# Kernel optimization log

Hardware: AMD Instinct MI355X
Metric: run time of the kernel (lower is better)

Reference implementation:

```python
import jax, jax.numpy as jnp
import numpy as np

B, S, D, H = 4, 2048, 1024, 16
PD = D // H  # projection (head) dim


def setup_inputs() -> dict:
    key = jax.random.key(0)
    ks = jax.random.split(key, 11)
    s = 1.0 / np.sqrt(D)
    return {
        "q": jax.random.normal(ks[0], (B, S, D), jnp.float32),
        "k": jax.random.normal(ks[1], (B, S, D), jnp.float32),
        "v": jax.random.normal(ks[2], (B, S, D), jnp.float32),
        "Wq": jax.random.normal(ks[3], (D, D), jnp.float32) * s,
        "bq": jnp.zeros((D,), jnp.float32),
        "Wk": jax.random.normal(ks[4], (D, D), jnp.float32) * s,
        "bk": jnp.zeros((D,), jnp.float32),
        "Wv": jax.random.normal(ks[5], (D, D), jnp.float32) * s,
        "bv": jnp.zeros((D,), jnp.float32),
        "Wo": jax.random.normal(ks[6], (D, D), jnp.float32) * s,
        "bo": jnp.zeros((D,), jnp.float32),
        "use_causal_mask": 1,
    }


def _split_heads(x):
    # [B,S,D] -> [B,H,S,PD]
    return x.reshape(B, S, H, PD).transpose(0, 2, 1, 3)


def reference(q, k, v, Wq, bq, Wk, bk, Wv, bv, Wo, bo, use_causal_mask):
    qh = _split_heads(q @ Wq + bq)
    kh = _split_heads(k @ Wk + bk)
    vh = _split_heads(v @ Wv + bv)
    # scaled dot-product attention, O(S^2) scores materialized as in original
    logits = jnp.einsum("bhsd,bhtd->bhst", qh, kh) / jnp.sqrt(jnp.float32(PD))
    if use_causal_mask:
        # Faithful to original (buggy) mask: band_part lower-tri ones, then
        # logits += log(mask*1e-6 + 1.0) -- adds ~1e-6 where allowed, 0 where masked.
        mask = jnp.tril(jnp.ones((S, S), jnp.float32))
        logits = logits + jnp.log(mask * 1e-6 + 1.0)
    attn = jax.nn.softmax(logits, axis=-1)
    out = jnp.einsum("bhst,bhtd->bhsd", attn, vh)
    concat = out.transpose(0, 2, 1, 3).reshape(B, S, D)
    return concat @ Wo + bo
```

## Files before the change

kernel.cpp:

```cpp
#include <hip/hip_runtime.h>

#define B_ 4
#define S_ 2048
#define D_ 1024
#define H_ 16
#define PD_ 64
#define M_ 8192
#define QSCALE 0.180336880145787f

typedef __attribute__((ext_vector_type(8))) short s16x8;
typedef __attribute__((ext_vector_type(4))) short s16x4;
typedef __attribute__((ext_vector_type(4))) float f32x4;

__device__ __forceinline__ short f2bf(float f) {
    unsigned int u = __float_as_uint(f);
    u = (u + 0x7FFFu + ((u >> 16) & 1u)) >> 16;
    return (short)u;
}

__device__ __forceinline__ unsigned int cvt_pk_bf16(float lo, float hi) {
    unsigned int r;
    asm("v_cvt_pk_bf16_f32 %0, %1, %2" : "=v"(r) : "v"(lo), "v"(hi));
    return r;
}

#if __has_builtin(__builtin_amdgcn_exp2f)
__device__ __forceinline__ float fast_exp2(float x) { return __builtin_amdgcn_exp2f(x); }
#else
__device__ __forceinline__ float fast_exp2(float x) {
    float r;
    asm("v_exp_f32 %0, %1" : "=v"(r) : "v"(x));
    return r;
}
#endif

#define MFMA(a, b, c) __builtin_amdgcn_mfma_f32_16x16x32_bf16(a, b, c, 0, 0, 0)

#if __has_builtin(__builtin_amdgcn_mfma_f32_16x16x16bf16_1k)
__device__ __forceinline__ f32x4 MFMA16(s16x4 a, s16x4 b, f32x4 c) {
    return __builtin_amdgcn_mfma_f32_16x16x16bf16_1k(a, b, c, 0, 0, 0);
}
#elif __has_builtin(__builtin_amdgcn_mfma_f32_16x16x16_bf16)
typedef __attribute__((ext_vector_type(4))) __bf16 bf16x4;
__device__ __forceinline__ f32x4 MFMA16(s16x4 a, s16x4 b, f32x4 c) {
    union UA { s16x4 s; bf16x4 b; };
    UA ua, ub;
    ua.s = a; ub.s = b;
    return __builtin_amdgcn_mfma_f32_16x16x16_bf16(ua.b, ub.b, c, 0, 0, 0);
}
#else
__device__ __forceinline__ f32x4 MFMA16(s16x4 a, s16x4 b, f32x4 c) {
    asm volatile("s_nop 1\n\tv_mfma_f32_16x16x16_bf16 %0, %1, %2, %0\n\ts_nop 7\n\ts_nop 7"
                 : "+v"(c) : "v"(a), "v"(b));
    return c;
}
#endif

__device__ __forceinline__ void gload16(const short* g, short* l) {
    __builtin_amdgcn_global_load_lds(
        (const __attribute__((address_space(1))) void*)g,
        (__attribute__((address_space(3))) void*)l, 16, 0, 0);
}

__global__ __launch_bounds__(256) void cvt_kernel(
    const float* __restrict__ q, const float* __restrict__ k, const float* __restrict__ v,
    short* __restrict__ oq, short* __restrict__ ok, short* __restrict__ ov) {
    const int z = blockIdx.z;
    const float* X = (z == 0) ? q : (z == 1) ? k : v;
    short* out = (z == 0) ? oq : (z == 1) ? ok : ov;
    const float s = (z == 0) ? QSCALE : 1.0f;
    size_t i0 = ((size_t)blockIdx.x * 256 + threadIdx.x) * 8;
    const size_t stride = (size_t)1024 * 256 * 8;
#pragma unroll
    for (int it = 0; it < 4; it++, i0 += stride) {
        float4 f0 = *(const float4*)&X[i0];
        float4 f1 = *(const float4*)&X[i0 + 4];
        s16x8 o = {f2bf(f0.x * s), f2bf(f0.y * s), f2bf(f0.z * s), f2bf(f0.w * s),
                   f2bf(f1.x * s), f2bf(f1.y * s), f2bf(f1.z * s), f2bf(f1.w * s)};
        *(s16x8*)&out[i0] = o;
    }
}

__global__ void wt_kernel(const float* __restrict__ Wq, const float* __restrict__ Wk,
                          const float* __restrict__ Wv, const float* __restrict__ Wo,
                          short* __restrict__ wt) {
    const float* W = (blockIdx.z == 0) ? Wq : (blockIdx.z == 1) ? Wk
                     : (blockIdx.z == 2) ? Wv : Wo;
    short* out = wt + (size_t)blockIdx.z * (D_ * D_);
    __shared__ float tile[32][33];
    const int k0 = blockIdx.x * 32, n0 = blockIdx.y * 32;
    const int tx = threadIdx.x, ty = threadIdx.y;
#pragma unroll
    for (int i = 0; i < 4; i++)
        tile[ty + 8 * i][tx] = W[(size_t)(k0 + ty + 8 * i) * D_ + n0 + tx];
    __syncthreads();
#pragma unroll
    for (int i = 0; i < 4; i++)
        out[(size_t)(n0 + ty + 8 * i) * D_ + k0 + tx] = f2bf(tile[tx][ty + 8 * i]);
}

__device__ __forceinline__ void gemm_core(const short* __restrict__ A,
                                          const short* __restrict__ Bm,
                                          int bm, int bn, short* lds,
                                          f32x4 acc[4][4]) {
    const int tid = threadIdx.x;
    const int lane = tid & 63, wid = tid >> 6;
    const int wr = (wid >> 1) * 64, wc = (wid & 1) * 64;
    const int l15 = lane & 15, l4 = lane >> 4;

    const int rr = tid >> 2;
    const int cc = tid & 3;
    const int csw = (cc ^ ((rr >> 1) & 3)) * 8;
    const short* ap = A + (size_t)(bm + rr) * D_ + csw;
    const short* bp = Bm + (size_t)(bn + rr) * D_ + csw;
    const int ldw = wid * 512;

    const int ard = (l4 ^ ((l15 >> 1) & 3)) * 8;

#define PSTAGE(bi, kkc)                                                  \
    do {                                                                 \
        short* Lp = lds + (bi) * 8192;                                   \
        gload16(ap + (kkc), Lp + ldw);                                   \
        gload16(ap + (size_t)64 * D_ + (kkc), Lp + 2048 + ldw);          \
        gload16(bp + (kkc), Lp + 4096 + ldw);                            \
        gload16(bp + (size_t)64 * D_ + (kkc), Lp + 6144 + ldw);          \
    } while (0)

    PSTAGE(0, 0);
    PSTAGE(1, 32);

    int cur = 0;
    for (int t = 0; t < 32; t++) {
        if (t + 2 < 32) {
            int nb = cur + 2;
            if (nb >= 3) nb -= 3;
            PSTAGE(nb, (t + 2) * 32);
        }
        if (t <= 29)
            asm volatile("s_waitcnt vmcnt(8)" ::: "memory");
        else if (t == 30)
            asm volatile("s_waitcnt vmcnt(4)" ::: "memory");
        else
            asm volatile("s_waitcnt vmcnt(0)" ::: "memory");
        __builtin_amdgcn_s_barrier();

        const short* La = lds + cur * 8192;
        const short* Lb = La + 4096;
        s16x8 af[4], bf[4];
#pragma unroll
        for (int i = 0; i < 4; i++)
            af[i] = *(const s16x8*)&La[(wr + i * 16 + l15) * 32 + ard];
#pragma unroll
        for (int j = 0; j < 4; j++)
            bf[j] = *(const s16x8*)&Lb[(wc + j * 16 + l15) * 32 + ard];
#pragma unroll
        for (int i = 0; i < 4; i++)
#pragma unroll
            for (int j = 0; j < 4; j++)
                acc[i][j] = MFMA(bf[j], af[i], acc[i][j]);

        __builtin_amdgcn_s_barrier();
        cur = (cur == 2) ? 0 : cur + 1;
    }
#undef PSTAGE
}

__global__ __launch_bounds__(256) void proj_kernel(
    const short* __restrict__ xq, const short* __restrict__ xk, const short* __restrict__ xv,
    const float* __restrict__ bq, const float* __restrict__ bk, const float* __restrict__ bv,
    const short* __restrict__ wtbase, short* __restrict__ outQ, short* __restrict__ outK,
    short* __restrict__ outVT) {
    const int id = blockIdx.x;
    const int xcd = id & 7, slot = id >> 3;
    const int sb = xcd + 8 * (slot >> 6);
    const int wi = slot & 63;
    const int z = sb >> 3;
    const int bn = (wi & 7) * 128;
    const int bm = (((sb & 7) << 3) + (wi >> 3)) * 128;

    const short* A = (z == 0) ? xq : (z == 1) ? xk : xv;
    const float* bias = (z == 0) ? bq : (z == 1) ? bk : bv;
    const short* Wt = wtbase + (size_t)z * (D_ * D_);
    const float bscale = (z == 0) ? QSCALE : 1.0f;

    __shared__ __align__(16) short lds[3 * 8192];

    const int tid = threadIdx.x;
    const int lane = tid & 63, wid = tid >> 6;
    const int wr = (wid >> 1) * 64, wc = (wid & 1) * 64;
    const int l15 = lane & 15, l4 = lane >> 4;

    f32x4 acc[4][4];
#pragma unroll
    for (int i = 0; i < 4; i++)
#pragma unroll
        for (int j = 0; j < 4; j++) acc[i][j] = (f32x4){0.f, 0.f, 0.f, 0.f};

    gemm_core(A, Wt, bm, bn, lds, acc);

    if (z == 2) {
        const int b = bm >> 11, sbase = bm & (S_ - 1);
        short* T = lds;
        for (int chunk = 0; chunk < 4; chunk++) {
            __syncthreads();
            if ((wc >> 6) == (chunk >> 1)) {
                const int jbase = (chunk & 1) * 2;
#pragma unroll
                for (int jj = 0; jj < 2; jj++) {
                    const int j = jbase + jj;
                    float4 b4 = *(const float4*)&bias[bn + wc + j * 16 + l4 * 4];
                    const int prow = jj * 16 + l4 * 4;
#pragma unroll
                    for (int i = 0; i < 4; i++) {
                        const int sc2 = wr + i * 16 + l15;
                        T[(prow + 0) * 132 + sc2] = f2bf(acc[i][j][0] + b4.x);
                        T[(prow + 1) * 132 + sc2] = f2bf(acc[i][j][1] + b4.y);
                        T[(prow + 2) * 132 + sc2] = f2bf(acc[i][j][2] + b4.z);
                        T[(prow + 3) * 132 + sc2] = f2bf(acc[i][j][3] + b4.w);
                    }
                }
            }
            __syncthreads();
#pragma unroll
            for (int pass = 0; pass < 2; pass++) {
                const int r = pass * 16 + (tid >> 4);
                const int sc3 = (tid & 15) * 8;
                s16x8 vv = *(const s16x8*)&T[r * 132 + sc3];
                const int grow = b * 1024 + bn + chunk * 32 + r;
                const int kvg = sc3 & 64;
                const int c8 = (sc3 >> 3) & 7;
                const int posA = ((2 * c8) & 3) * 16 + (c8 >> 1) * 4;
                const int posB = ((2 * c8 + 1) & 3) * 16 + (c8 >> 1) * 4;
                const int sx = (r & 7) << 3;
                const s16x4* hv = (const s16x4*)&vv;
                const size_t base = (size_t)grow * S_ + sbase + kvg;
                *(s16x4*)&outVT[base + (posA ^ sx)] = hv[0];
                *(s16x4*)&outVT[base + (posB ^ sx)] = hv[1];
            }
        }
    } else {
        short* out = (z == 0) ? outQ : outK;
#pragma unroll
        for (int i = 0; i < 4; i++) {
            const int m = bm + wr + i * 16 + l15;
            const int b = m >> 11, s = m & (S_ - 1);
#pragma unroll
            for (int j = 0; j < 4; j++) {
                const int n = bn + wc + j * 16 + l4 * 4;
                float4 b4 = *(const float4*)&bias[n];
                s16x4 st;
                st[0] = f2bf(acc[i][j][0] + b4.x * bscale);
                st[1] = f2bf(acc[i][j][1] + b4.y * bscale);
                st[2] = f2bf(acc[i][j][2] + b4.z * bscale);
                st[3] = f2bf(acc[i][j][3] + b4.w * bscale);
                const int h = n >> 6, pd = n & 63;
                const int pdsw = (z == 1) ? (pd ^ ((s & 7) << 3)) : pd;
                *(s16x4*)&out[(((size_t)(b * H_ + h)) * S_ + s) * PD_ + pdsw] = st;
            }
        }
    }
}

__global__ __launch_bounds__(512, 4) void attn_kernel(
    const short* __restrict__ Qh, const short* __restrict__ Kh,
    const short* __restrict__ Vtg, short* __restrict__ aout) {
    const int did = blockIdx.x + gridDim.x * blockIdx.y;
    const int bh = (did & 7) * 8 + ((did >> 3) & 7);
    const int q0 = (did >> 6) * 128;
    const short* Qp = Qh + (size_t)bh * (S_ * PD_);
    const short* Kp = Kh + (size_t)bh * (S_ * PD_);
    const short* Vp = Vtg + (size_t)bh * (PD_ * S_);

    const int tid = threadIdx.x;
    const int lane = tid & 63, w = tid >> 6;
    const int l15 = lane & 15, l4 = lane >> 4;
    const int swz = (l15 & 7) << 3;

    __shared__ __align__(16) short Ks[3][64 * 64];
    __shared__ __align__(16) short Vs[3][64 * 64];

    s16x8 qf[2];
#pragma unroll
    for (int kk = 0; kk < 2; kk++)
        qf[kk] = *(const s16x8*)&Qp[(size_t)(q0 + w * 16 + l15) * PD_ + kk * 32 + l4 * 8];

    const s16x4 ones = {(short)0x3F80, (short)0x3F80, (short)0x3F80, (short)0x3F80};

    f32x4 oacc[4];
#pragma unroll
    for (int i = 0; i < 4; i++) oacc[i] = (f32x4){0.f, 0.f, 0.f, 0.f};
    f32x4 sacc = (f32x4){0.f, 0.f, 0.f, 0.f};

    const short* kbase = Kp + (size_t)(tid >> 3) * PD_ + (tid & 7) * 8;
    const short* vbase = Vp + (size_t)(tid >> 3) * S_ + (tid & 7) * 8;
    const int ldw = w * 512;

#define AISSUE(bsel, st)                                              \
    do {                                                              \
        gload16(kbase + (size_t)(st) * (64 * PD_), &Ks[bsel][ldw]);   \
        gload16(vbase + (st) * 64, &Vs[bsel][ldw]);                   \
    } while (0)

    AISSUE(0, 0);
    AISSUE(1, 1);

    int cur = 0;
    for (int t = 0; t < 32; t++) {
        if (t < 31)
            asm volatile("s_waitcnt vmcnt(2)" ::: "memory");
        else
            asm volatile("s_waitcnt vmcnt(0)" ::: "memory");
        __syncthreads();
        if (t + 2 < 32) {
            int nb = cur + 2;
            if (nb >= 3) nb -= 3;
            AISSUE(nb, t + 2);
        }
        const short* Kc = Ks[cur];
        const short* Vc = Vs[cur];

        f32x4 s4[4];
#pragma unroll
        for (int n4 = 0; n4 < 4; n4++) s4[n4] = (f32x4){0.f, 0.f, 0.f, 0.f};
        __builtin_amdgcn_s_setprio(1);
#pragma unroll
        for (int n4 = 0; n4 < 4; n4++)
#pragma unroll
            for (int kk = 0; kk < 2; kk++) {
                s16x8 kf = *(const s16x8*)&Kc[(n4 * 16 + l15) * 64 + ((kk * 32 + l4 * 8) ^ swz)];
                s4[n4] = MFMA(kf, qf[kk], s4[n4]);
            }
        __builtin_amdgcn_s_setprio(0);

        s16x4 pf[4];
#pragma unroll
        for (int n4 = 0; n4 < 4; n4++) {
            float p0 = fast_exp2(s4[n4][0]);
            float p1 = fast_exp2(s4[n4][1]);
            float p2 = fast_exp2(s4[n4][2]);
            float p3 = fast_exp2(s4[n4][3]);
            uint2 pw;
            pw.x = cvt_pk_bf16(p0, p1);
            pw.y = cvt_pk_bf16(p2, p3);
            pf[n4] = *(s16x4*)&pw;
            sacc = MFMA16(ones, pf[n4], sacc);
        }

        __builtin_amdgcn_s_setprio(1);
#pragma unroll
        for (int i = 0; i < 4; i++) {
            const int vrow = (i * 16 + l15) * 64;
            s16x8 rv1 = *(const s16x8*)&Vc[vrow + (((l4 * 2) ^ (l15 & 7)) << 3)];
            s16x8 rv2 = *(const s16x8*)&Vc[vrow + (((l4 * 2 + 1) ^ (l15 & 7)) << 3)];
            const s16x4* h1 = (const s16x4*)&rv1;
            const s16x4* h2 = (const s16x4*)&rv2;
            oacc[i] = MFMA16(h1[0], pf[0], oacc[i]);
            oacc[i] = MFMA16(h1[1], pf[1], oacc[i]);
            oacc[i] = MFMA16(h2[0], pf[2], oacc[i]);
            oacc[i] = MFMA16(h2[1], pf[3], oacc[i]);
        }
        __builtin_amdgcn_s_setprio(0);
        cur = (cur == 2) ? 0 : cur + 1;
    }
#undef AISSUE

    const float inv = 1.0f / sacc[0];
    const int qrow = q0 + w * 16 + l15;
    const int bb = bh >> 4, hh = bh & 15;
#pragma unroll
    for (int i = 0; i < 4; i++) {
        s16x4 st;
        st[0] = f2bf(oacc[i][0] * inv);
        st[1] = f2bf(oacc[i][1] * inv);
        st[2] = f2bf(oacc[i][2] * inv);
        st[3] = f2bf(oacc[i][3] * inv);
        *(s16x4*)&aout[((size_t)(bb * S_ + qrow)) * D_ + hh * PD_ + i * 16 + l4 * 4] = st;
    }
}

__global__ __launch_bounds__(256) void out_kernel(
    const short* __restrict__ A, const short* __restrict__ Wt,
    const float* __restrict__ bo, float* __restrict__ out) {
    __shared__ __align__(16) short lds[3 * 8192];

    const int bm = blockIdx.x * 128, bn = blockIdx.y * 128;
    const int tid = threadIdx.x;
    const int lane = tid & 63, wid = tid >> 6;
    const int wr = (wid >> 1) * 64, wc = (wid & 1) * 64;
    const int l15 = lane & 15, l4 = lane >> 4;

    f32x4 acc[4][4];
#pragma unroll
    for (int i = 0; i < 4; i++)
#pragma unroll
        for (int j = 0; j < 4; j++) acc[i][j] = (f32x4){0.f, 0.f, 0.f, 0.f};

    gemm_core(A, Wt, bm, bn, lds, acc);

#pragma unroll
    for (int i = 0; i < 4; i++) {
        const int m = bm + wr + i * 16 + l15;
#pragma unroll
        for (int j = 0; j < 4; j++) {
            const int n = bn + wc + j * 16 + l4 * 4;
            float4 b4 = *(const float4*)&bo[n];
            float4 st;
            st.x = acc[i][j][0] + b4.x;
            st.y = acc[i][j][1] + b4.y;
            st.z = acc[i][j][2] + b4.z;
            st.w = acc[i][j][3] + b4.w;
            *(float4*)&out[(size_t)m * D_ + n] = st;
        }
    }
}

extern "C" void kernel_launch(void* const* d_in, const int* in_sizes, int n_in,
                              void* d_out, int out_size, void* d_ws, size_t ws_size,
                              hipStream_t stream) {
    const float* q  = (const float*)d_in[0];
    const float* k  = (const float*)d_in[1];
    const float* v  = (const float*)d_in[2];
    const float* Wq = (const float*)d_in[3];
    const float* bq = (const float*)d_in[4];
    const float* Wk = (const float*)d_in[5];
    const float* bk = (const float*)d_in[6];
    const float* Wv = (const float*)d_in[7];
    const float* bv = (const float*)d_in[8];
    const float* Wo = (const float*)d_in[9];
    const float* bo = (const float*)d_in[10];

    const size_t TEN = (size_t)M_ * D_;
    short* ws  = (short*)d_ws;
    short* wt  = ws;
    short* qh  = ws + 4 * (size_t)D_ * D_;
    short* kh  = qh + TEN;
    short* vtg = kh + TEN;
    short* xbk = vtg + TEN;
    short* xbv = xbk + TEN;
    short* xbq = (short*)d_out;
    short* ao  = xbk;
    float* out = (float*)d_out;

    hipLaunchKernelGGL(cvt_kernel, dim3(1024, 1, 3), dim3(256, 1, 1), 0, stream,
                       q, k, v, xbq, xbk, xbv);
    hipLaunchKernelGGL(wt_kernel, dim3(32, 32, 4), dim3(32, 8, 1), 0, stream,
                       Wq, Wk, Wv, Wo, wt);
    hipLaunchKernelGGL(proj_kernel, dim3(1536, 1, 1), dim3(256, 1, 1), 0, stream,
                       xbq, xbk, xbv, bq, bk, bv, wt, qh, kh, vtg);
    hipLaunchKernelGGL(attn_kernel, dim3(16, 64, 1), dim3(512, 1, 1), 0, stream,
                       qh, kh, vtg, ao);
    hipLaunchKernelGGL(out_kernel, dim3(64, 8, 1), dim3(256, 1, 1), 0, stream,
                       ao, wt + (size_t)3 * D_ * D_, bo, out);
}
```

Measured before the change: 236.7 us.

## Use 16x16x32 MFMA for PV and row-sum, merge prep kernels

Replaces the 16x16x16 bf16 MFMAs in the attention P·V and softmax-denominator steps with 16x16x32 MFMAs. The P fragments are packed into 8-element vectors, and the V-transpose store layout in the projection kernel is permuted to match the new operand layout. This halves the MFMA instruction count in the inner loop and simplifies the V LDS reads. Separately, the input-conversion and weight-transpose kernels are fused into one launch to cut launch overhead. The layout change must stay consistent between the projection and attention kernels.

New measurement: 229.4 us. 3.1% less time.

```diff
diff --git a/kernel.cpp b/kernel.cpp
--- a/kernel.cpp
+++ b/kernel.cpp
@@ -36,67 +36,52 @@
 
 #define MFMA(a, b, c) __builtin_amdgcn_mfma_f32_16x16x32_bf16(a, b, c, 0, 0, 0)
 
-#if __has_builtin(__builtin_amdgcn_mfma_f32_16x16x16bf16_1k)
-__device__ __forceinline__ f32x4 MFMA16(s16x4 a, s16x4 b, f32x4 c) {
-    return __builtin_amdgcn_mfma_f32_16x16x16bf16_1k(a, b, c, 0, 0, 0);
-}
-#elif __has_builtin(__builtin_amdgcn_mfma_f32_16x16x16_bf16)
-typedef __attribute__((ext_vector_type(4))) __bf16 bf16x4;
-__device__ __forceinline__ f32x4 MFMA16(s16x4 a, s16x4 b, f32x4 c) {
-    union UA { s16x4 s; bf16x4 b; };
-    UA ua, ub;
-    ua.s = a; ub.s = b;
-    return __builtin_amdgcn_mfma_f32_16x16x16_bf16(ua.b, ub.b, c, 0, 0, 0);
-}
-#else
-__device__ __forceinline__ f32x4 MFMA16(s16x4 a, s16x4 b, f32x4 c) {
-    asm volatile("s_nop 1\n\tv_mfma_f32_16x16x16_bf16 %0, %1, %2, %0\n\ts_nop 7\n\ts_nop 7"
-                 : "+v"(c) : "v"(a), "v"(b));
-    return c;
-}
-#endif
-
 __device__ __forceinline__ void gload16(const short* g, short* l) {
     __builtin_amdgcn_global_load_lds(
         (const __attribute__((address_space(1))) void*)g,
         (__attribute__((address_space(3))) void*)l, 16, 0, 0);
 }
 
-__global__ __launch_bounds__(256) void cvt_kernel(
+__global__ __launch_bounds__(256) void prep_kernel(
     const float* __restrict__ q, const float* __restrict__ k, const float* __restrict__ v,
-    short* __restrict__ oq, short* __restrict__ ok, short* __restrict__ ov) {
-    const int z = blockIdx.z;
-    const float* X = (z == 0) ? q : (z == 1) ? k : v;
-    short* out = (z == 0) ? oq : (z == 1) ? ok : ov;
-    const float s = (z == 0) ? QSCALE : 1.0f;
-    size_t i0 = ((size_t)blockIdx.x * 256 + threadIdx.x) * 8;
-    const size_t stride = (size_t)1024 * 256 * 8;
-#pragma unroll
-    for (int it = 0; it < 4; it++, i0 += stride) {
-        float4 f0 = *(const float4*)&X[i0];
-        float4 f1 = *(const float4*)&X[i0 + 4];
-        s16x8 o = {f2bf(f0.x * s), f2bf(f0.y * s), f2bf(f0.z * s), f2bf(f0.w * s),
-                   f2bf(f1.x * s), f2bf(f1.y * s), f2bf(f1.z * s), f2bf(f1.w * s)};
-        *(s16x8*)&out[i0] = o;
-    }
-}
-
-__global__ void wt_kernel(const float* __restrict__ Wq, const float* __restrict__ Wk,
-                          const float* __restrict__ Wv, const float* __restrict__ Wo,
-                          short* __restrict__ wt) {
-    const float* W = (blockIdx.z == 0) ? Wq : (blockIdx.z == 1) ? Wk
-                     : (blockIdx.z == 2) ? Wv : Wo;
-    short* out = wt + (size_t)blockIdx.z * (D_ * D_);
+    const float* __restrict__ Wq, const float* __restrict__ Wk,
+    const float* __restrict__ Wv, const float* __restrict__ Wo,
+    short* __restrict__ oq, short* __restrict__ ok, short* __restrict__ ov,
+    short* __restrict__ wt) {
     __shared__ float tile[32][33];
-    const int k0 = blockIdx.x * 32, n0 = blockIdx.y * 32;
-    const int tx = threadIdx.x, ty = threadIdx.y;
-#pragma unroll
-    for (int i = 0; i < 4; i++)
-        tile[ty + 8 * i][tx] = W[(size_t)(k0 + ty + 8 * i) * D_ + n0 + tx];
-    __syncthreads();
-#pragma unroll
-    for (int i = 0; i < 4; i++)
-        out[(size_t)(n0 + ty + 8 * i) * D_ + k0 + tx] = f2bf(tile[tx][ty + 8 * i]);
+    const int id = blockIdx.x;
+    const int tid = threadIdx.x;
+    if (id < 3072) {
+        const int z = id >> 10, x = id & 1023;
+        const float* X = (z == 0) ? q : (z == 1) ? k : v;
+        short* out = (z == 0) ? oq : (z == 1) ? ok : ov;
+        const float s = (z == 0) ? QSCALE : 1.0f;
+        size_t i0 = ((size_t)x * 256 + tid) * 8;
+        const size_t stride = (size_t)1024 * 256 * 8;
+#pragma unroll
+        for (int it = 0; it < 4; it++, i0 += stride) {
+            float4 f0 = *(const float4*)&X[i0];
+            float4 f1 = *(const float4*)&X[i0 + 4];
+            s16x8 o = {f2bf(f0.x * s), f2bf(f0.y * s), f2bf(f0.z * s), f2bf(f0.w * s),
+                       f2bf(f1.x * s), f2bf(f1.y * s), f2bf(f1.z * s), f2bf(f1.w * s)};
+            *(s16x8*)&out[i0] = o;
+        }
+    } else {
+        int t = id - 3072;
+        const int z = t >> 10;
+        t &= 1023;
+        const float* W = (z == 0) ? Wq : (z == 1) ? Wk : (z == 2) ? Wv : Wo;
+        short* out = wt + (size_t)z * (D_ * D_);
+        const int k0 = (t >> 5) * 32, n0 = (t & 31) * 32;
+        const int tx = tid & 31, ty = tid >> 5;
+#pragma unroll
+        for (int i = 0; i < 4; i++)
+            tile[ty + 8 * i][tx] = W[(size_t)(k0 + ty + 8 * i) * D_ + n0 + tx];
+        __syncthreads();
+#pragma unroll
+        for (int i = 0; i < 4; i++)
+            out[(size_t)(n0 + ty + 8 * i) * D_ + k0 + tx] = f2bf(tile[tx][ty + 8 * i]);
+    }
 }
 
 __device__ __forceinline__ void gemm_core(const short* __restrict__ A,
@@ -229,8 +214,10 @@
                 const int grow = b * 1024 + bn + chunk * 32 + r;
                 const int kvg = sc3 & 64;
                 const int c8 = (sc3 >> 3) & 7;
-                const int posA = ((2 * c8) & 3) * 16 + (c8 >> 1) * 4;
-                const int posB = ((2 * c8 + 1) & 3) * 16 + (c8 >> 1) * 4;
+                const int hh2 = (c8 >> 2) * 32;
+                const int m4 = ((c8 >> 1) & 1) * 4;
+                const int posA = hh2 + 8 * ((2 * c8) & 3) + m4;
+                const int posB = hh2 + 8 * ((2 * c8 + 1) & 3) + m4;
                 const int sx = (r & 7) << 3;
                 const s16x4* hv = (const s16x4*)&vv;
                 const size_t base = (size_t)grow * S_ + sbase + kvg;
@@ -284,7 +271,8 @@
     for (int kk = 0; kk < 2; kk++)
         qf[kk] = *(const s16x8*)&Qp[(size_t)(q0 + w * 16 + l15) * PD_ + kk * 32 + l4 * 8];
 
-    const s16x4 ones = {(short)0x3F80, (short)0x3F80, (short)0x3F80, (short)0x3F80};
+    const s16x8 ones8 = {(short)0x3F80, (short)0x3F80, (short)0x3F80, (short)0x3F80,
+                         (short)0x3F80, (short)0x3F80, (short)0x3F80, (short)0x3F80};
 
     f32x4 oacc[4];
 #pragma unroll
@@ -332,32 +320,34 @@
             }
         __builtin_amdgcn_s_setprio(0);
 
-        s16x4 pf[4];
-#pragma unroll
-        for (int n4 = 0; n4 < 4; n4++) {
-            float p0 = fast_exp2(s4[n4][0]);
-            float p1 = fast_exp2(s4[n4][1]);
-            float p2 = fast_exp2(s4[n4][2]);
-            float p3 = fast_exp2(s4[n4][3]);
-            uint2 pw;
-            pw.x = cvt_pk_bf16(p0, p1);
-            pw.y = cvt_pk_bf16(p2, p3);
-            pf[n4] = *(s16x4*)&pw;
-            sacc = MFMA16(ones, pf[n4], sacc);
+        s16x8 pb[2];
+#pragma unroll
+        for (int h = 0; h < 2; h++) {
+            float p0 = fast_exp2(s4[2 * h][0]);
+            float p1 = fast_exp2(s4[2 * h][1]);
+            float p2 = fast_exp2(s4[2 * h][2]);
+            float p3 = fast_exp2(s4[2 * h][3]);
+            float p4 = fast_exp2(s4[2 * h + 1][0]);
+            float p5 = fast_exp2(s4[2 * h + 1][1]);
+            float p6 = fast_exp2(s4[2 * h + 1][2]);
+            float p7 = fast_exp2(s4[2 * h + 1][3]);
+            union { uint4 u; s16x8 s; } pu;
+            pu.u.x = cvt_pk_bf16(p0, p1);
+            pu.u.y = cvt_pk_bf16(p2, p3);
+            pu.u.z = cvt_pk_bf16(p4, p5);
+            pu.u.w = cvt_pk_bf16(p6, p7);
+            pb[h] = pu.s;
+            sacc = MFMA(ones8, pb[h], sacc);
         }
 
         __builtin_amdgcn_s_setprio(1);
 #pragma unroll
         for (int i = 0; i < 4; i++) {
             const int vrow = (i * 16 + l15) * 64;
-            s16x8 rv1 = *(const s16x8*)&Vc[vrow + (((l4 * 2) ^ (l15 & 7)) << 3)];
-            s16x8 rv2 = *(const s16x8*)&Vc[vrow + (((l4 * 2 + 1) ^ (l15 & 7)) << 3)];
-            const s16x4* h1 = (const s16x4*)&rv1;
-            const s16x4* h2 = (const s16x4*)&rv2;
-            oacc[i] = MFMA16(h1[0], pf[0], oacc[i]);
-            oacc[i] = MFMA16(h1[1], pf[1], oacc[i]);
-            oacc[i] = MFMA16(h2[0], pf[2], oacc[i]);
-            oacc[i] = MFMA16(h2[1], pf[3], oacc[i]);
+            s16x8 v0 = *(const s16x8*)&Vc[vrow + ((8 * l4) ^ swz)];
+            s16x8 v1 = *(const s16x8*)&Vc[vrow + ((32 + 8 * l4) ^ swz)];
+            oacc[i] = MFMA(v0, pb[0], oacc[i]);
+            oacc[i] = MFMA(v1, pb[1], oacc[i]);
         }
         __builtin_amdgcn_s_setprio(0);
         cur = (cur == 2) ? 0 : cur + 1;
@@ -441,10 +431,8 @@
     short* ao  = xbk;
     float* out = (float*)d_out;
 
-    hipLaunchKernelGGL(cvt_kernel, dim3(1024, 1, 3), dim3(256, 1, 1), 0, stream,
-                       q, k, v, xbq, xbk, xbv);
-    hipLaunchKernelGGL(wt_kernel, dim3(32, 32, 4), dim3(32, 8, 1), 0, stream,
-                       Wq, Wk, Wv, Wo, wt);
+    hipLaunchKernelGGL(prep_kernel, dim3(7168, 1, 1), dim3(256, 1, 1), 0, stream,
+                       q, k, v, Wq, Wk, Wv, Wo, xbq, xbk, xbv, wt);
     hipLaunchKernelGGL(proj_kernel, dim3(1536, 1, 1), dim3(256, 1, 1), 0, stream,
                        xbq, xbk, xbv, bq, bk, bv, wt, qh, kh, vtg);
     hipLaunchKernelGGL(attn_kernel, dim3(16, 64, 1), dim3(512, 1, 1), 0, stream,
```
